# Kernel optimization log

Measured on AMD Instinct MI355X. Metric: run time of the kernel, lower is better.

Reference implementation:

```python
import jax, jax.numpy as jnp
import numpy as np

B = 64           # batch size
N = 512          # number of nodes
E = 1            # edge feature dims of the GSO
M = 256          # nodes carrying edge-variant weights (hybrid EV since M < N)
F = [1, 8, 8]    # node-signal features per layer
K = [3, 3]       # shift taps per layer
MLP = [512, 128] # readout dims
P_EDGE = 0.03    # graph density
ZTOL = 1e-9      # zero tolerance for sparsity pattern


def setup_inputs():
    ks = jax.random.split(jax.random.key(0), 13)
    x = jax.random.normal(ks[0], (B, F[0], N), dtype=jnp.float32)
    adj = (jax.random.uniform(ks[1], (E, N, N)) < P_EDGE).astype(jnp.float32)
    S = adj * jax.random.normal(ks[2], (E, N, N), dtype=jnp.float32) / np.sqrt(N * P_EDGE)

    def w(k, shape, scale):
        return jax.random.normal(k, shape, dtype=jnp.float32) * np.float32(scale)

    wEV1 = w(ks[3], (F[1], E, K[0], F[0], N, N), 1.0 / np.sqrt(F[0] * N))
    wLSI1 = w(ks[4], (F[1], E, K[0], F[0]), 1.0 / np.sqrt(F[0] * K[0]))
    b1 = w(ks[5], (F[1], 1), 0.1)
    wEV2 = w(ks[6], (F[2], E, K[1], F[1], N, N), 1.0 / np.sqrt(F[1] * N))
    wLSI2 = w(ks[7], (F[2], E, K[1], F[1]), 1.0 / np.sqrt(F[1] * K[1]))
    b2 = w(ks[8], (F[2], 1), 0.1)
    W1 = w(ks[9], (MLP[0], F[2] * N), 1.0 / np.sqrt(F[2] * N))
    bW1 = w(ks[10], (MLP[0],), 0.1)
    W2 = w(ks[11], (MLP[1], MLP[0]), 1.0 / np.sqrt(MLP[0]))
    bW2 = w(ks[12], (MLP[1],), 0.1)
    return dict(x=x, S=S, wEV1=wEV1, wLSI1=wLSI1, b1=b1,
                wEV2=wEV2, wLSI2=wLSI2, b2=b2, W1=W1, bW1=bW1, W2=W2, bW2=bW2)


def _sparsity_mask(S):
    # support of S + I, then kill the [M:, M:] block (hybrid EV mask)
    eye = jnp.eye(N, dtype=S.dtype)
    sp = ((jnp.abs(S) + eye[None]) > ZTOL).astype(S.dtype)      # (E,N,N)
    hyb = jnp.ones((N, N), S.dtype).at[M:, M:].set(0.0)
    return sp * hyb[None]


def _ev_layer(xl, S, sp, wEV, wLSI, b):
    # xl: (B,G,N); wEV: (F,E,K,G,N,N); wLSI: (F,E,K,G); b: (F,1)
    Phi = wEV * sp[None, :, None, None]                          # masked filter matrices
    Kl = wEV.shape[2]
    # EV part: y = sum_k Phi^(k) ... Phi^(0) x, summed over e, g
    z = jnp.einsum('fegmn,bgn->bfegm', Phi[:, :, 0], xl)
    y = z
    for k in range(1, Kl):
        z = jnp.einsum('fegmn,bfegn->bfegm', Phi[:, :, k], z)
        y = y + z
    y = y.sum(axis=(2, 3))                                       # (B,F,N)
    # LSI part of the hybrid filter: sum_{e,k,g} h_{fekg} S_e^k x_g
    xe = jnp.broadcast_to(xl[:, None], (xl.shape[0], S.shape[0]) + xl.shape[1:])
    zs = [xe]                                                    # k = 0: identity
    for k in range(1, Kl):
        zs.append(jnp.einsum('emn,begn->begm', S, zs[-1]))
    zst = jnp.stack(zs, axis=2)                                  # (B,E,K,G,N)
    y = y + jnp.einsum('fekg,bekgn->bfn', wLSI, zst)
    return y + b[None]                                           # bias broadcast over nodes


def reference(x, S, wEV1, wLSI1, b1, wEV2, wLSI2, b2, W1, bW1, W2, bW2):
    sp = _sparsity_mask(S)
    # order=None -> permIdentity, so x[:, :, order] == x; NoPool is identity
    y = _ev_layer(x, S, sp, wEV1, wLSI1, b1)
    y = _ev_layer(y, S, sp, wEV2, wLSI2, b2)
    yf = y.reshape(y.shape[0], -1)                               # (B, F[-1]*N)
    h = yf @ W1.T + bW1                                          # linear MLP (no activation)
    return h @ W2.T + bW2
```

## Files before the change

### kernel.cpp

```cpp
#include <hip/hip_runtime.h>
#include <cstdint>
#include <cstddef>

#define NNODE 512
#define MMASK 256
#define ZT 1e-9f
#define NPL 216

__global__ __launch_bounds__(256) void k_prep(const float* __restrict__ x,
                                              const float* __restrict__ S,
                                              int* __restrict__ sp_col, int* __restrict__ sp_cnt,
                                              int* __restrict__ s_col, float* __restrict__ s_val,
                                              int* __restrict__ s_cnt,
                                              float* __restrict__ xt) {
  int gtid = blockIdx.x * 256 + threadIdx.x;
  int W = gtid >> 6, lane = threadIdx.x & 63;
  {
    int n = gtid >> 6, b = gtid & 63;
    xt[gtid] = x[b * NNODE + n];
  }
  int m = W;
  int csp = 0, cs = 0;
  unsigned long long lt = (1ull << lane) - 1ull;
  for (int ch = 0; ch < 8; ++ch) {
    int n = ch * 64 + lane;
    float s = S[m * NNODE + n];
    bool ps  = (s != 0.f);
    bool psp = ((fabsf(s) + ((m == n) ? 1.f : 0.f)) > ZT) && !((m >= MMASK) && (n >= MMASK));
    unsigned long long msp = __ballot(psp), ms = __ballot(ps);
    if (psp) { int p = csp + __popcll(msp & lt); if (p < 64) sp_col[(m << 6) + p] = n; }
    if (ps)  { int p = cs  + __popcll(ms  & lt); if (p < 64) { s_col[(m << 6) + p] = n; s_val[(m << 6) + p] = s; } }
    csp += __popcll(msp); cs += __popcll(ms);
  }
  if (lane >= csp) sp_col[(m << 6) + lane] = 0;
  if (lane >= cs)  { s_col[(m << 6) + lane] = 0; s_val[(m << 6) + lane] = 0.f; }
  if (lane == 0) { sp_cnt[m] = (csp < 64 ? csp : 64); s_cnt[m] = (cs < 64 ? cs : 64); }
}

__device__ __forceinline__ void pack_one(const float* __restrict__ src,
                                         const int* __restrict__ sp_col,
                                         const int* __restrict__ sp_cnt,
                                         float* __restrict__ wpk,
                                         int pidx, int r, int lane) {
  int cl = sp_col[(r << 6) + lane];
  int cnt = sp_cnt[r];
  float wl = (lane < cnt) ? src[cl] : 0.f;
  wpk[((size_t)pidx << 15) + (r << 6) + lane] = wl;
}

__device__ __forceinline__ float ell_mac_s(const int* __restrict__ cols,
                                           const float* __restrict__ ws,
                                           int cnt,
                                           const float* __restrict__ zin, int lane) {
  float a0 = 0.f, a1 = 0.f, a2 = 0.f, a3 = 0.f;
  for (int base = 0; base < cnt; base += 16) {
#pragma unroll
    for (int i = 0; i < 16; i += 4) {
      int   c0 = cols[base + i    ]; float w0 = ws[base + i    ];
      int   c1 = cols[base + i + 1]; float w1 = ws[base + i + 1];
      int   c2 = cols[base + i + 2]; float w2 = ws[base + i + 2];
      int   c3 = cols[base + i + 3]; float w3 = ws[base + i + 3];
      a0 += w0 * zin[(c0 << 6) + lane];
      a1 += w1 * zin[(c1 << 6) + lane];
      a2 += w2 * zin[(c2 << 6) + lane];
      a3 += w3 * zin[(c3 << 6) + lane];
    }
  }
  return (a0 + a1) + (a2 + a3);
}

__global__ __launch_bounds__(256) void k_packA(const float* __restrict__ wEV1,
                                               const int* __restrict__ sp_col,
                                               const int* __restrict__ sp_cnt,
                                               float* __restrict__ wpk) {
  int lane = threadIdx.x & 63;
  int W = __builtin_amdgcn_readfirstlane((blockIdx.x * 256 + (int)threadIdx.x) >> 6);
  int nwv = (gridDim.x << 2);
  for (int u = W; u < 24 * 512; u += nwv) {
    int p = u >> 9, r = u & 511;
    pack_one(wEV1 + ((size_t)p << 18) + (r << 9), sp_col, sp_cnt, wpk, p, r, lane);
  }
}

__global__ __launch_bounds__(256) void k_l1s0(const float* __restrict__ wEV2,
    const float* __restrict__ wpk,
    const int* __restrict__ sp_col, const int* __restrict__ sp_cnt,
    const int* __restrict__ s_col, const float* __restrict__ s_val, const int* __restrict__ s_cnt,
    const float* __restrict__ xt, float* __restrict__ zA1, float* __restrict__ u1,
    float* __restrict__ wpk_out) {
  int lane = threadIdx.x & 63;
  int W = __builtin_amdgcn_readfirstlane((blockIdx.x * 256 + (int)threadIdx.x) >> 6);
  int nwv = (gridDim.x << 2);
  for (int u = W; u < 4608 + 32768; u += nwv) {
    if (u < 4096) {
      int f = u >> 9, r = u & 511;
      zA1[((size_t)f << 15) + (r << 6) + lane] =
          ell_mac_s(sp_col + (r << 6), wpk + ((size_t)(f * 3 + 0) << 15) + (r << 6),
                    sp_cnt[r], xt, lane);
    } else if (u < 4608) {
      int r = u - 4096;
      u1[(r << 6) + lane] =
          ell_mac_s(s_col + (r << 6), s_val + (r << 6), s_cnt[r], xt, lane);
    } else {
      int jj = u - 4608;
      int p2 = jj >> 9, r = jj & 511;
      pack_one(wEV2 + ((size_t)p2 << 18) + (r << 9), sp_col, sp_cnt,
               wpk_out, 24 + p2, r, lane);
    }
  }
}

__global__ __launch_bounds__(256) void k_l1s1(const float* __restrict__ wEV2,
    const float* __restrict__ wpk,
    const int* __restrict__ sp_col, const int* __restrict__ sp_cnt,
    const int* __restrict__ s_col, const float* __restrict__ s_val, const int* __restrict__ s_cnt,
    const float* __restrict__ zA1, const float* __restrict__ u1,
    float* __restrict__ zB1, float* __restrict__ u2,
    float* __restrict__ wpk_out) {
  int lane = threadIdx.x & 63;
  int W = __builtin_amdgcn_readfirstlane((blockIdx.x * 256 + (int)threadIdx.x) >> 6);
  int nwv = (gridDim.x << 2);
  for (int u = W; u < 4608 + 32768; u += nwv) {
    if (u < 4096) {
      int f = u >> 9, r = u & 511;
      zB1[((size_t)f << 15) + (r << 6) + lane] =
          ell_mac_s(sp_col + (r << 6), wpk + ((size_t)(f * 3 + 1) << 15) + (r << 6),
                    sp_cnt[r], zA1 + ((size_t)f << 15), lane);
    } else if (u < 4608) {
      int r = u - 4096;
      u2[(r << 6) + lane] =
          ell_mac_s(s_col + (r << 6), s_val + (r << 6), s_cnt[r], u1, lane);
    } else {
      int jj = u - 4608 + 32768;
      int p2 = jj >> 9, r = jj & 511;
      pack_one(wEV2 + ((size_t)p2 << 18) + (r << 9), sp_col, sp_cnt,
               wpk_out, 24 + p2, r, lane);
    }
  }
}

__global__ __launch_bounds__(256) void k_l1s2(const float* __restrict__ wEV2,
    const float* __restrict__ wpk,
    const int* __restrict__ sp_col, const int* __restrict__ sp_cnt,
    const float* __restrict__ zA1, const float* __restrict__ zB1,
    const float* __restrict__ xt, const float* __restrict__ u1, const float* __restrict__ u2,
    const float* __restrict__ wLSI1, const float* __restrict__ b1, float* __restrict__ y1,
    float* __restrict__ wpk_out) {
  int lane = threadIdx.x & 63;
  int W = __builtin_amdgcn_readfirstlane((blockIdx.x * 256 + (int)threadIdx.x) >> 6);
  int nwv = (gridDim.x << 2);
  for (int u = W; u < 4096 + 32768; u += nwv) {
    if (u < 4096) {
      int f = u >> 9, r = u & 511;
      float a = ell_mac_s(sp_col + (r << 6), wpk + ((size_t)(f * 3 + 2) << 15) + (r << 6),
                          sp_cnt[r], zB1 + ((size_t)f << 15), lane);
      int idx = (r << 6) + lane;
      size_t fi = ((size_t)f << 15) + idx;
      y1[fi] = zA1[fi] + zB1[fi] + a
             + wLSI1[f * 3 + 0] * xt[idx] + wLSI1[f * 3 + 1] * u1[idx]
             + wLSI1[f * 3 + 2] * u2[idx] + b1[f];
    } else {
      int jj = u - 4096 + 65536;
      int p2 = jj >> 9, r = jj & 511;
      pack_one(wEV2 + ((size_t)p2 << 18) + (r << 9), sp_col, sp_cnt,
               wpk_out, 24 + p2, r, lane);
    }
  }
}

__global__ __launch_bounds__(256) void k_l2s0(const float* __restrict__ wpk,
    const int* __restrict__ sp_col, const int* __restrict__ sp_cnt,
    const int* __restrict__ s_col, const float* __restrict__ s_val, const int* __restrict__ s_cnt,
    const float* __restrict__ y1, float* __restrict__ zA2, float* __restrict__ v1) {
  int lane = threadIdx.x & 63;
  int W = __builtin_amdgcn_readfirstlane((blockIdx.x * 256 + (int)threadIdx.x) >> 6);
  int nwv = (gridDim.x << 2);
  for (int u = W; u < 36864; u += nwv) {
    if (u < 32768) {
      int c = u >> 9, r = u & 511;
      int f = c >> 3, g = c & 7;
      zA2[((size_t)c << 15) + (r << 6) + lane] =
          ell_mac_s(sp_col + (r << 6),
                    wpk + ((size_t)(24 + (f * 3 + 0) * 8 + g) << 15) + (r << 6),
                    sp_cnt[r], y1 + ((size_t)g << 15), lane);
    } else {
      int t = u - 32768;
      int g = t >> 9, r = t & 511;
      v1[((size_t)g << 15) + (r << 6) + lane] =
          ell_mac_s(s_col + (r << 6), s_val + (r << 6), s_cnt[r],
                    y1 + ((size_t)g << 15), lane);
    }
  }
}

__global__ __launch_bounds__(256) void k_l2s1(const float* __restrict__ wpk,
    const int* __restrict__ sp_col, const int* __restrict__ sp_cnt,
    const int* __restrict__ s_col, const float* __restrict__ s_val, const int* __restrict__ s_cnt,
    const float* __restrict__ zA2, const float* __restrict__ v1,
    float* __restrict__ zB2, float* __restrict__ v2) {
  int lane = threadIdx.x & 63;
  int W = __builtin_amdgcn_readfirstlane((blockIdx.x * 256 + (int)threadIdx.x) >> 6);
  int nwv = (gridDim.x << 2);
  for (int u = W; u < 36864; u += nwv) {
    if (u < 32768) {
      int c = u >> 9, r = u & 511;
      int f = c >> 3, g = c & 7;
      zB2[((size_t)c << 15) + (r << 6) + lane] =
          ell_mac_s(sp_col + (r << 6),
                    wpk + ((size_t)(24 + (f * 3 + 1) * 8 + g) << 15) + (r << 6),
                    sp_cnt[r], zA2 + ((size_t)c << 15), lane);
    } else {
      int t = u - 32768;
      int g = t >> 9, r = t & 511;
      v2[((size_t)g << 15) + (r << 6) + lane] =
          ell_mac_s(s_col + (r << 6), s_val + (r << 6), s_cnt[r],
                    v1 + ((size_t)g << 15), lane);
    }
  }
}

__global__ __launch_bounds__(256) void k_l2s2(const float* __restrict__ wpk,
    const int* __restrict__ sp_col, const int* __restrict__ sp_cnt,
    const float* __restrict__ zA2, const float* __restrict__ zB2,
    const float* __restrict__ y1, const float* __restrict__ v1, const float* __restrict__ v2,
    const float* __restrict__ wLSI2, const float* __restrict__ b2,
    const float* __restrict__ bW1, float* __restrict__ y2, float* __restrict__ ht) {
  int gtid = blockIdx.x * 256 + threadIdx.x;
  int lane = threadIdx.x & 63;
  int W = __builtin_amdgcn_readfirstlane(gtid >> 6);
  int nwv = (gridDim.x << 2);
  if (gtid < 32768) ht[gtid] = bW1[gtid >> 6];
  for (int u = W; u < 4096; u += nwv) {
    int f = u >> 9, r = u & 511;
    int idx = (r << 6) + lane;
    const int* cols = sp_col + (r << 6);
    int cnt = sp_cnt[r];
    float acc = b2[f];
#pragma unroll
    for (int g = 0; g < 8; ++g) {
      int c = f * 8 + g;
      float a = ell_mac_s(cols,
                          wpk + ((size_t)(24 + (f * 3 + 2) * 8 + g) << 15) + (r << 6),
                          cnt, zB2 + ((size_t)c << 15), lane);
      size_t ci = ((size_t)c << 15) + idx;
      size_t gi = ((size_t)g << 15) + idx;
      acc += zA2[ci] + zB2[ci] + a
           + wLSI2[f * 24 + g]      * y1[gi]
           + wLSI2[f * 24 + 8 + g]  * v1[gi]
           + wLSI2[f * 24 + 16 + g] * v2[gi];
    }
    y2[((size_t)f << 15) + idx] = acc;
  }
}

__global__ __launch_bounds__(256) void k_gemm1(const float* __restrict__ W1,
                                               const float* __restrict__ y2,
                                               const float* __restrict__ bW2,
                                               float* __restrict__ ht,
                                               float* __restrict__ out) {
  int gtid = blockIdx.x * 256 + threadIdx.x;
  int lane = threadIdx.x & 63;
  int W = __builtin_amdgcn_readfirstlane(gtid >> 6);
  int nwv = (gridDim.x << 2);
  if (gtid < 8192) out[gtid] = bW2[gtid & 127];
  for (int u = W; u < 512; u += nwv) {
    int pg = u >> 3, ks = u & 7;
    const float* wrow = W1 + (size_t)pg * 8 * 4096 + ks * 512;
    const float* yb = y2 + ((size_t)(ks * 512) << 6);
    float acc[8] = {0, 0, 0, 0, 0, 0, 0, 0};
    for (int q = 0; q < 512; q += 8) {
      float yv[8];
#pragma unroll
      for (int i = 0; i < 8; ++i) yv[i] = yb[((q + i) << 6) + lane];
#pragma unroll
      for (int i = 0; i < 8; ++i) {
#pragma unroll
        for (int p = 0; p < 8; ++p) acc[p] += wrow[(size_t)p * 4096 + q + i] * yv[i];
      }
    }
#pragma unroll
    for (int p = 0; p < 8; ++p) atomicAdd(&ht[((pg * 8 + p) << 6) + lane], acc[p]);
  }
}

__global__ __launch_bounds__(256) void k_gemm2(const float* __restrict__ W2,
                                               const float* __restrict__ ht,
                                               float* __restrict__ out) {
  int lane = threadIdx.x & 63;
  int W = __builtin_amdgcn_readfirstlane((blockIdx.x * 256 + (int)threadIdx.x) >> 6);
  int nwv = (gridDim.x << 2);
  for (int u = W; u < 1024; u += nwv) {
    int o = u >> 3, qs = u & 7;
    const float* w2 = W2 + (size_t)o * 512 + qs * 64;
    const float* hb = ht + ((size_t)(qs * 64) << 6);
    float acc = 0.f;
    for (int q = 0; q < 64; q += 8) {
#pragma unroll
      for (int i = 0; i < 8; ++i) acc += w2[q + i] * hb[((q + i) << 6) + lane];
    }
    atomicAdd(&out[lane * 128 + o], acc);
  }
}

extern "C" void kernel_launch(void* const* d_in, const int* in_sizes, int n_in,
                              void* d_out, int out_size, void* d_ws, size_t ws_size,
                              hipStream_t stream) {
  const float* x     = (const float*)d_in[0];
  const float* S     = (const float*)d_in[1];
  const float* wEV1  = (const float*)d_in[2];
  const float* wLSI1 = (const float*)d_in[3];
  const float* b1    = (const float*)d_in[4];
  const float* wEV2  = (const float*)d_in[5];
  const float* wLSI2 = (const float*)d_in[6];
  const float* b2    = (const float*)d_in[7];
  const float* W1    = (const float*)d_in[8];
  const float* bW1   = (const float*)d_in[9];
  const float* W2    = (const float*)d_in[10];
  const float* bW2   = (const float*)d_in[11];
  float* out = (float*)d_out;

  char* w = (char*)d_ws;
  auto alloc = [&](size_t bytes) { char* p = w; w += (bytes + 255) & ~(size_t)255; return p; };
  int*   sp_col = (int*)alloc(512 * 64 * 4);
  int*   sp_cnt = (int*)alloc(512 * 4);
  int*   s_col  = (int*)alloc(512 * 64 * 4);
  float* s_val  = (float*)alloc(512 * 64 * 4);
  int*   s_cnt  = (int*)alloc(512 * 4);
  float* wpk    = (float*)alloc((size_t)NPL * 32768 * 4);
  float* xt     = (float*)alloc((size_t)32768 * 4);
  float* u1     = (float*)alloc((size_t)32768 * 4);
  float* u2     = (float*)alloc((size_t)32768 * 4);
  float* zA1    = (float*)alloc((size_t)8 * 32768 * 4);
  float* zB1    = (float*)alloc((size_t)8 * 32768 * 4);
  float* y1     = (float*)alloc((size_t)8 * 32768 * 4);
  float* zA2    = (float*)alloc((size_t)64 * 32768 * 4);
  float* zB2    = (float*)alloc((size_t)64 * 32768 * 4);
  float* v1     = (float*)alloc((size_t)8 * 32768 * 4);
  float* v2     = (float*)alloc((size_t)8 * 32768 * 4);
  float* y2     = (float*)alloc((size_t)8 * 32768 * 4);
  float* ht     = (float*)alloc((size_t)32768 * 4);
  (void)ws_size; (void)in_sizes; (void)n_in; (void)out_size;

  k_prep<<<128, 256, 0, stream>>>(x, S, sp_col, sp_cnt, s_col, s_val, s_cnt, xt);
  k_packA<<<3072, 256, 0, stream>>>(wEV1, sp_col, sp_cnt, wpk);
  k_l1s0<<<9344, 256, 0, stream>>>(wEV2, wpk, sp_col, sp_cnt, s_col, s_val, s_cnt, xt, zA1, u1, wpk);
  k_l1s1<<<9344, 256, 0, stream>>>(wEV2, wpk, sp_col, sp_cnt, s_col, s_val, s_cnt, zA1, u1, zB1, u2, wpk);
  k_l1s2<<<9216, 256, 0, stream>>>(wEV2, wpk, sp_col, sp_cnt, zA1, zB1, xt, u1, u2, wLSI1, b1, y1, wpk);
  k_l2s0<<<9216, 256, 0, stream>>>(wpk, sp_col, sp_cnt, s_col, s_val, s_cnt, y1, zA2, v1);
  k_l2s1<<<9216, 256, 0, stream>>>(wpk, sp_col, sp_cnt, s_col, s_val, s_cnt, zA2, v1, zB2, v2);
  k_l2s2<<<1024, 256, 0, stream>>>(wpk, sp_col, sp_cnt, zA2, zB2, y1, v1, v2, wLSI2, b2, bW1, y2, ht);
  k_gemm1<<<128, 256, 0, stream>>>(W1, y2, bW2, ht, out);
  k_gemm2<<<256, 256, 0, stream>>>(W2, ht, out);
}
```

Measured before the change: 396.6 us.

## Batch multiple filters per wave in ELL SpMV stages and weight packing

Each wave now handles several output filters (or input channels) for one row, so the column indices and gathered input values are loaded once and reused across 4–8 accumulators instead of being refetched per filter. Weight packing processes four filter planes per wave, sharing the column and count loads. Grid sizes shrink to match the reduced work-item counts. This trades more registers per wave and less parallelism for fewer redundant gathers.

```diff
diff --git a/kernel.cpp b/kernel.cpp
--- a/kernel.cpp
+++ b/kernel.cpp
@@ -37,17 +37,6 @@
   if (lane == 0) { sp_cnt[m] = (csp < 64 ? csp : 64); s_cnt[m] = (cs < 64 ? cs : 64); }
 }
 
-__device__ __forceinline__ void pack_one(const float* __restrict__ src,
-                                         const int* __restrict__ sp_col,
-                                         const int* __restrict__ sp_cnt,
-                                         float* __restrict__ wpk,
-                                         int pidx, int r, int lane) {
-  int cl = sp_col[(r << 6) + lane];
-  int cnt = sp_cnt[r];
-  float wl = (lane < cnt) ? src[cl] : 0.f;
-  wpk[((size_t)pidx << 15) + (r << 6) + lane] = wl;
-}
-
 __device__ __forceinline__ float ell_mac_s(const int* __restrict__ cols,
                                            const float* __restrict__ ws,
                                            int cnt,
@@ -76,9 +65,16 @@
   int lane = threadIdx.x & 63;
   int W = __builtin_amdgcn_readfirstlane((blockIdx.x * 256 + (int)threadIdx.x) >> 6);
   int nwv = (gridDim.x << 2);
-  for (int u = W; u < 24 * 512; u += nwv) {
-    int p = u >> 9, r = u & 511;
-    pack_one(wEV1 + ((size_t)p << 18) + (r << 9), sp_col, sp_cnt, wpk, p, r, lane);
+  for (int u = W; u < 6 * 512; u += nwv) {
+    int p4 = u >> 9, r = u & 511;
+    int cl = sp_col[(r << 6) + lane];
+    int cnt = sp_cnt[r];
+    const float* s0 = wEV1 + ((size_t)(p4 * 4) << 18) + (r << 9);
+#pragma unroll
+    for (int t = 0; t < 4; ++t) {
+      float wl = (lane < cnt) ? s0[((size_t)t << 18) + cl] : 0.f;
+      wpk[((size_t)(p4 * 4 + t) << 15) + (r << 6) + lane] = wl;
+    }
   }
 }
 
@@ -91,21 +87,44 @@
   int lane = threadIdx.x & 63;
   int W = __builtin_amdgcn_readfirstlane((blockIdx.x * 256 + (int)threadIdx.x) >> 6);
   int nwv = (gridDim.x << 2);
-  for (int u = W; u < 4608 + 32768; u += nwv) {
-    if (u < 4096) {
-      int f = u >> 9, r = u & 511;
-      zA1[((size_t)f << 15) + (r << 6) + lane] =
-          ell_mac_s(sp_col + (r << 6), wpk + ((size_t)(f * 3 + 0) << 15) + (r << 6),
-                    sp_cnt[r], xt, lane);
-    } else if (u < 4608) {
-      int r = u - 4096;
+  for (int u = W; u < 1024 + 8192; u += nwv) {
+    if (u < 512) {
+      int r = u;
+      const int* cols = sp_col + (r << 6);
+      int cnt = sp_cnt[r];
+      float acc[8] = {0, 0, 0, 0, 0, 0, 0, 0};
+      for (int base = 0; base < cnt; base += 16) {
+#pragma unroll
+        for (int i = 0; i < 16; i += 4) {
+          int c0 = cols[base + i], c1 = cols[base + i + 1];
+          int c2 = cols[base + i + 2], c3 = cols[base + i + 3];
+          float z0 = xt[(c0 << 6) + lane], z1 = xt[(c1 << 6) + lane];
+          float z2 = xt[(c2 << 6) + lane], z3 = xt[(c3 << 6) + lane];
+#pragma unroll
+          for (int f = 0; f < 8; ++f) {
+            const float* wf = wpk + ((size_t)(f * 3) << 15) + (r << 6);
+            acc[f] += wf[base + i] * z0 + wf[base + i + 1] * z1
+                    + wf[base + i + 2] * z2 + wf[base + i + 3] * z3;
+          }
+        }
+      }
+#pragma unroll
+      for (int f = 0; f < 8; ++f) zA1[((size_t)f << 15) + (r << 6) + lane] = acc[f];
+    } else if (u < 1024) {
+      int r = u - 512;
       u1[(r << 6) + lane] =
           ell_mac_s(s_col + (r << 6), s_val + (r << 6), s_cnt[r], xt, lane);
     } else {
-      int jj = u - 4608;
-      int p2 = jj >> 9, r = jj & 511;
-      pack_one(wEV2 + ((size_t)p2 << 18) + (r << 9), sp_col, sp_cnt,
-               wpk_out, 24 + p2, r, lane);
+      int jj = u - 1024;
+      int p4 = jj >> 9, r = jj & 511;
+      int cl = sp_col[(r << 6) + lane];
+      int cnt = sp_cnt[r];
+      const float* s0 = wEV2 + ((size_t)(p4 * 4) << 18) + (r << 9);
+#pragma unroll
+      for (int t = 0; t < 4; ++t) {
+        float wl = (lane < cnt) ? s0[((size_t)t << 18) + cl] : 0.f;
+        wpk_out[((size_t)(24 + p4 * 4 + t) << 15) + (r << 6) + lane] = wl;
+      }
     }
   }
 }
@@ -120,21 +139,47 @@
   int lane = threadIdx.x & 63;
   int W = __builtin_amdgcn_readfirstlane((blockIdx.x * 256 + (int)threadIdx.x) >> 6);
   int nwv = (gridDim.x << 2);
-  for (int u = W; u < 4608 + 32768; u += nwv) {
-    if (u < 4096) {
-      int f = u >> 9, r = u & 511;
-      zB1[((size_t)f << 15) + (r << 6) + lane] =
-          ell_mac_s(sp_col + (r << 6), wpk + ((size_t)(f * 3 + 1) << 15) + (r << 6),
-                    sp_cnt[r], zA1 + ((size_t)f << 15), lane);
-    } else if (u < 4608) {
-      int r = u - 4096;
+  for (int u = W; u < 1536 + 8192; u += nwv) {
+    if (u < 1024) {
+      int fp = u >> 9, r = u & 511;
+      const int* cols = sp_col + (r << 6);
+      int cnt = sp_cnt[r];
+      float acc[4] = {0, 0, 0, 0};
+      for (int base = 0; base < cnt; base += 16) {
+#pragma unroll
+        for (int i = 0; i < 16; i += 4) {
+          int c0 = cols[base + i], c1 = cols[base + i + 1];
+          int c2 = cols[base + i + 2], c3 = cols[base + i + 3];
+#pragma unroll
+          for (int q = 0; q < 4; ++q) {
+            int f = fp * 4 + q;
+            const float* wf = wpk + ((size_t)(f * 3 + 1) << 15) + (r << 6);
+            const float* zq = zA1 + ((size_t)f << 15);
+            acc[q] += wf[base + i]     * zq[(c0 << 6) + lane]
+                    + wf[base + i + 1] * zq[(c1 << 6) + lane]
+                    + wf[base + i + 2] * zq[(c2 << 6) + lane]
+                    + wf[base + i + 3] * zq[(c3 << 6) + lane];
+          }
+        }
+      }
+#pragma unroll
+      for (int q = 0; q < 4; ++q)
+        zB1[((size_t)(fp * 4 + q) << 15) + (r << 6) + lane] = acc[q];
+    } else if (u < 1536) {
+      int r = u - 1024;
       u2[(r << 6) + lane] =
           ell_mac_s(s_col + (r << 6), s_val + (r << 6), s_cnt[r], u1, lane);
     } else {
-      int jj = u - 4608 + 32768;
-      int p2 = jj >> 9, r = jj & 511;
-      pack_one(wEV2 + ((size_t)p2 << 18) + (r << 9), sp_col, sp_cnt,
-               wpk_out, 24 + p2, r, lane);
+      int jj = u - 1536;
+      int p4 = jj >> 9, r = jj & 511;
+      int cl = sp_col[(r << 6) + lane];
+      int cnt = sp_cnt[r];
+      const float* s0 = wEV2 + ((size_t)(64 + p4 * 4) << 18) + (r << 9);
+#pragma unroll
+      for (int t = 0; t < 4; ++t) {
+        float wl = (lane < cnt) ? s0[((size_t)t << 18) + cl] : 0.f;
+        wpk_out[((size_t)(24 + 64 + p4 * 4 + t) << 15) + (r << 6) + lane] = wl;
+      }
     }
   }
 }
@@ -149,21 +194,50 @@
   int lane = threadIdx.x & 63;
   int W = __builtin_amdgcn_readfirstlane((blockIdx.x * 256 + (int)threadIdx.x) >> 6);
   int nwv = (gridDim.x << 2);
-  for (int u = W; u < 4096 + 32768; u += nwv) {
-    if (u < 4096) {
-      int f = u >> 9, r = u & 511;
-      float a = ell_mac_s(sp_col + (r << 6), wpk + ((size_t)(f * 3 + 2) << 15) + (r << 6),
-                          sp_cnt[r], zB1 + ((size_t)f << 15), lane);
+  for (int u = W; u < 1024 + 8192; u += nwv) {
+    if (u < 1024) {
+      int fp = u >> 9, r = u & 511;
+      const int* cols = sp_col + (r << 6);
+      int cnt = sp_cnt[r];
+      float acc[4] = {0, 0, 0, 0};
+      for (int base = 0; base < cnt; base += 16) {
+#pragma unroll
+        for (int i = 0; i < 16; i += 4) {
+          int c0 = cols[base + i], c1 = cols[base + i + 1];
+          int c2 = cols[base + i + 2], c3 = cols[base + i + 3];
+#pragma unroll
+          for (int q = 0; q < 4; ++q) {
+            int f = fp * 4 + q;
+            const float* wf = wpk + ((size_t)(f * 3 + 2) << 15) + (r << 6);
+            const float* zq = zB1 + ((size_t)f << 15);
+            acc[q] += wf[base + i]     * zq[(c0 << 6) + lane]
+                    + wf[base + i + 1] * zq[(c1 << 6) + lane]
+                    + wf[base + i + 2] * zq[(c2 << 6) + lane]
+                    + wf[base + i + 3] * zq[(c3 << 6) + lane];
+          }
+        }
+      }
       int idx = (r << 6) + lane;
-      size_t fi = ((size_t)f << 15) + idx;
-      y1[fi] = zA1[fi] + zB1[fi] + a
-             + wLSI1[f * 3 + 0] * xt[idx] + wLSI1[f * 3 + 1] * u1[idx]
-             + wLSI1[f * 3 + 2] * u2[idx] + b1[f];
+      float xv = xt[idx], u1v = u1[idx], u2v = u2[idx];
+#pragma unroll
+      for (int q = 0; q < 4; ++q) {
+        int f = fp * 4 + q;
+        size_t fi = ((size_t)f << 15) + idx;
+        y1[fi] = zA1[fi] + zB1[fi] + acc[q]
+               + wLSI1[f * 3 + 0] * xv + wLSI1[f * 3 + 1] * u1v
+               + wLSI1[f * 3 + 2] * u2v + b1[f];
+      }
     } else {
-      int jj = u - 4096 + 65536;
-      int p2 = jj >> 9, r = jj & 511;
-      pack_one(wEV2 + ((size_t)p2 << 18) + (r << 9), sp_col, sp_cnt,
-               wpk_out, 24 + p2, r, lane);
+      int jj = u - 1024;
+      int p4 = jj >> 9, r = jj & 511;
+      int cl = sp_col[(r << 6) + lane];
+      int cnt = sp_cnt[r];
+      const float* s0 = wEV2 + ((size_t)(128 + p4 * 4) << 18) + (r << 9);
+#pragma unroll
+      for (int t = 0; t < 4; ++t) {
+        float wl = (lane < cnt) ? s0[((size_t)t << 18) + cl] : 0.f;
+        wpk_out[((size_t)(24 + 128 + p4 * 4 + t) << 15) + (r << 6) + lane] = wl;
+      }
     }
   }
 }
@@ -175,20 +249,52 @@
   int lane = threadIdx.x & 63;
   int W = __builtin_amdgcn_readfirstlane((blockIdx.x * 256 + (int)threadIdx.x) >> 6);
   int nwv = (gridDim.x << 2);
-  for (int u = W; u < 36864; u += nwv) {
-    if (u < 32768) {
-      int c = u >> 9, r = u & 511;
-      int f = c >> 3, g = c & 7;
-      zA2[((size_t)c << 15) + (r << 6) + lane] =
-          ell_mac_s(sp_col + (r << 6),
-                    wpk + ((size_t)(24 + (f * 3 + 0) * 8 + g) << 15) + (r << 6),
-                    sp_cnt[r], y1 + ((size_t)g << 15), lane);
+  for (int u = W; u < 4608; u += nwv) {
+    if (u < 4096) {
+      int g = u >> 9, r = u & 511;
+      const int* cols = sp_col + (r << 6);
+      int cnt = sp_cnt[r];
+      const float* zin = y1 + ((size_t)g << 15);
+      float acc[8] = {0, 0, 0, 0, 0, 0, 0, 0};
+      for (int base = 0; base < cnt; base += 16) {
+#pragma unroll
+        for (int i = 0; i < 16; i += 4) {
+          int c0 = cols[base + i], c1 = cols[base + i + 1];
+          int c2 = cols[base + i + 2], c3 = cols[base + i + 3];
+          float z0 = zin[(c0 << 6) + lane], z1 = zin[(c1 << 6) + lane];
+          float z2 = zin[(c2 << 6) + lane], z3 = zin[(c3 << 6) + lane];
+#pragma unroll
+          for (int f = 0; f < 8; ++f) {
+            const float* wf = wpk + ((size_t)(24 + (f * 3) * 8 + g) << 15) + (r << 6);
+            acc[f] += wf[base + i] * z0 + wf[base + i + 1] * z1
+                    + wf[base + i + 2] * z2 + wf[base + i + 3] * z3;
+          }
+        }
+      }
+#pragma unroll
+      for (int f = 0; f < 8; ++f)
+        zA2[((size_t)(f * 8 + g) << 15) + (r << 6) + lane] = acc[f];
     } else {
-      int t = u - 32768;
-      int g = t >> 9, r = t & 511;
-      v1[((size_t)g << 15) + (r << 6) + lane] =
-          ell_mac_s(s_col + (r << 6), s_val + (r << 6), s_cnt[r],
-                    y1 + ((size_t)g << 15), lane);
+      int r = u - 4096;
+      const int* cols = s_col + (r << 6);
+      const float* vals = s_val + (r << 6);
+      int cnt = s_cnt[r];
+      float acc[8] = {0, 0, 0, 0, 0, 0, 0, 0};
+      for (int base = 0; base < cnt; base += 16) {
+#pragma unroll
+        for (int i = 0; i < 16; i += 2) {
+          int c0 = cols[base + i], c1 = cols[base + i + 1];
+          float w0 = vals[base + i], w1 = vals[base + i + 1];
+#pragma unroll
+          for (int g = 0; g < 8; ++g) {
+            const float* zg = y1 + ((size_t)g << 15);
+            acc[g] += w0 * zg[(c0 << 6) + lane] + w1 * zg[(c1 << 6) + lane];
+          }
+        }
+      }
+#pragma unroll
+      for (int g = 0; g < 8; ++g)
+        v1[((size_t)g << 15) + (r << 6) + lane] = acc[g];
     }
   }
 }
@@ -201,20 +307,50 @@
   int lane = threadIdx.x & 63;
   int W = __builtin_amdgcn_readfirstlane((blockIdx.x * 256 + (int)threadIdx.x) >> 6);
   int nwv = (gridDim.x << 2);
-  for (int u = W; u < 36864; u += nwv) {
-    if (u < 32768) {
-      int c = u >> 9, r = u & 511;
-      int f = c >> 3, g = c & 7;
-      zB2[((size_t)c << 15) + (r << 6) + lane] =
-          ell_mac_s(sp_col + (r << 6),
-                    wpk + ((size_t)(24 + (f * 3 + 1) * 8 + g) << 15) + (r << 6),
-                    sp_cnt[r], zA2 + ((size_t)c << 15), lane);
+  for (int u = W; u < 4608; u += nwv) {
+    if (u < 4096) {
+      int f = u >> 9, r = u & 511;
+      const int* cols = sp_col + (r << 6);
+      int cnt = sp_cnt[r];
+      const float* zb = zA2 + ((size_t)(f * 8) << 15);
+      float acc[8] = {0, 0, 0, 0, 0, 0, 0, 0};
+      for (int base = 0; base < cnt; base += 16) {
+#pragma unroll
+        for (int i = 0; i < 16; i += 2) {
+          int c0 = cols[base + i], c1 = cols[base + i + 1];
+#pragma unroll
+          for (int g = 0; g < 8; ++g) {
+            const float* wf = wpk + ((size_t)(24 + (f * 3 + 1) * 8 + g) << 15) + (r << 6);
+            const float* zg = zb + ((size_t)g << 15);
+            acc[g] += wf[base + i]     * zg[(c0 << 6) + lane]
+                    + wf[base + i + 1] * zg[(c1 << 6) + lane];
+          }
+        }
+      }
+#pragma unroll
+      for (int g = 0; g < 8; ++g)
+        zB2[((size_t)(f * 8 + g) << 15) + (r << 6) + lane] = acc[g];
     } else {
-      int t = u - 32768;
-      int g = t >> 9, r = t & 511;
-      v2[((size_t)g << 15) + (r << 6) + lane] =
-          ell_mac_s(s_col + (r << 6), s_val + (r << 6), s_cnt[r],
-                    v1 + ((size_t)g << 15), lane);
+      int r = u - 4096;
+      const int* cols = s_col + (r << 6);
+      const float* vals = s_val + (r << 6);
+      int cnt = s_cnt[r];
+      float acc[8] = {0, 0, 0, 0, 0, 0, 0, 0};
+      for (int base = 0; base < cnt; base += 16) {
+#pragma unroll
+        for (int i = 0; i < 16; i += 2) {
+          int c0 = cols[base + i], c1 = cols[base + i + 1];
+          float w0 = vals[base + i], w1 = vals[base + i + 1];
+#pragma unroll
+          for (int g = 0; g < 8; ++g) {
+            const float* zg = v1 + ((size_t)g << 15);
+            acc[g] += w0 * zg[(c0 << 6) + lane] + w1 * zg[(c1 << 6) + lane];
+          }
+        }
+      }
+#pragma unroll
+      for (int g = 0; g < 8; ++g)
+        v2[((size_t)g << 15) + (r << 6) + lane] = acc[g];
     }
   }
 }
@@ -235,16 +371,28 @@
     int idx = (r << 6) + lane;
     const int* cols = sp_col + (r << 6);
     int cnt = sp_cnt[r];
+    const float* zb = zB2 + ((size_t)(f * 8) << 15);
+    float acc8[8] = {0, 0, 0, 0, 0, 0, 0, 0};
+    for (int base = 0; base < cnt; base += 16) {
+#pragma unroll
+      for (int i = 0; i < 16; i += 2) {
+        int c0 = cols[base + i], c1 = cols[base + i + 1];
+#pragma unroll
+        for (int g = 0; g < 8; ++g) {
+          const float* wf = wpk + ((size_t)(24 + (f * 3 + 2) * 8 + g) << 15) + (r << 6);
+          const float* zg = zb + ((size_t)g << 15);
+          acc8[g] += wf[base + i]     * zg[(c0 << 6) + lane]
+                   + wf[base + i + 1] * zg[(c1 << 6) + lane];
+        }
+      }
+    }
     float acc = b2[f];
 #pragma unroll
     for (int g = 0; g < 8; ++g) {
       int c = f * 8 + g;
-      float a = ell_mac_s(cols,
-                          wpk + ((size_t)(24 + (f * 3 + 2) * 8 + g) << 15) + (r << 6),
-                          cnt, zB2 + ((size_t)c << 15), lane);
       size_t ci = ((size_t)c << 15) + idx;
       size_t gi = ((size_t)g << 15) + idx;
-      acc += zA2[ci] + zB2[ci] + a
+      acc += zA2[ci] + zB2[ci] + acc8[g]
            + wLSI2[f * 24 + g]      * y1[gi]
            + wLSI2[f * 24 + 8 + g]  * v1[gi]
            + wLSI2[f * 24 + 16 + g] * v2[gi];
@@ -342,12 +490,12 @@
   (void)ws_size; (void)in_sizes; (void)n_in; (void)out_size;
 
   k_prep<<<128, 256, 0, stream>>>(x, S, sp_col, sp_cnt, s_col, s_val, s_cnt, xt);
-  k_packA<<<3072, 256, 0, stream>>>(wEV1, sp_col, sp_cnt, wpk);
-  k_l1s0<<<9344, 256, 0, stream>>>(wEV2, wpk, sp_col, sp_cnt, s_col, s_val, s_cnt, xt, zA1, u1, wpk);
-  k_l1s1<<<9344, 256, 0, stream>>>(wEV2, wpk, sp_col, sp_cnt, s_col, s_val, s_cnt, zA1, u1, zB1, u2, wpk);
-  k_l1s2<<<9216, 256, 0, stream>>>(wEV2, wpk, sp_col, sp_cnt, zA1, zB1, xt, u1, u2, wLSI1, b1, y1, wpk);
-  k_l2s0<<<9216, 256, 0, stream>>>(wpk, sp_col, sp_cnt, s_col, s_val, s_cnt, y1, zA2, v1);
-  k_l2s1<<<9216, 256, 0, stream>>>(wpk, sp_col, sp_cnt, s_col, s_val, s_cnt, zA2, v1, zB2, v2);
+  k_packA<<<768, 256, 0, stream>>>(wEV1, sp_col, sp_cnt, wpk);
+  k_l1s0<<<2304, 256, 0, stream>>>(wEV2, wpk, sp_col, sp_cnt, s_col, s_val, s_cnt, xt, zA1, u1, wpk);
+  k_l1s1<<<2432, 256, 0, stream>>>(wEV2, wpk, sp_col, sp_cnt, s_col, s_val, s_cnt, zA1, u1, zB1, u2, wpk);
+  k_l1s2<<<2304, 256, 0, stream>>>(wEV2, wpk, sp_col, sp_cnt, zA1, zB1, xt, u1, u2, wLSI1, b1, y1, wpk);
+  k_l2s0<<<1152, 256, 0, stream>>>(wpk, sp_col, sp_cnt, s_col, s_val, s_cnt, y1, zA2, v1);
+  k_l2s1<<<1152, 256, 0, stream>>>(wpk, sp_col, sp_cnt, s_col, s_val, s_cnt, zA2, v1, zB2, v2);
   k_l2s2<<<1024, 256, 0, stream>>>(wpk, sp_col, sp_cnt, zA2, zB2, y1, v1, v2, wLSI2, b2, bW1, y2, ht);
   k_gemm1<<<128, 256, 0, stream>>>(W1, y2, bW2, ht, out);
   k_gemm2<<<256, 256, 0, stream>>>(W2, ht, out);
```

Measured after the change: 411.8 us. 1.04x slower.
